# Optimization experiments

Hardware: AMD Instinct MI355X
Metric: run time of the kernel (lower is better)

Reference implementation:

```python
import jax, jax.numpy as jnp
import numpy as np
from jax import lax

# module hyperparams (from init_kwargs)
K = 7
STRIDE = 1
PAD = 3
DIL = 1


def setup_inputs() -> dict:
    key = jax.random.key(0)
    ks = jax.random.split(key, 5)
    B, Cin, Cout, L = 4, 256, 256, 8192
    x = jax.random.normal(ks[0], (B, Cin, L), jnp.float32)
    # main conv weight (Cout, Cin, K), kaiming-ish scale
    weight = jax.random.normal(ks[1], (Cout, Cin, K), jnp.float32) * (1.0 / np.sqrt(Cin * K))
    bias = jax.random.normal(ks[2], (Cout,), jnp.float32) * 0.01
    # offset conv: Conv1d(Cin -> K, kernel K); small values so sampling is perturbed but in-range
    offset_w = jax.random.normal(ks[3], (K, Cin, K), jnp.float32) * 0.01
    offset_b = jax.random.normal(ks[4], (K,), jnp.float32) * 0.01
    return {"x": x, "weight": weight, "bias": bias, "offset_w": offset_w, "offset_b": offset_b}


def reference(x, weight, bias, offset_w, offset_b):
    B, Cin, L = x.shape
    out_len = (L + 2 * PAD - DIL * (K - 1) - 1) // STRIDE + 1

    # offset conv: (B, Cin, L) -> (B, K, out_len)
    offsets = lax.conv_general_dilated(
        x, offset_w, window_strides=(STRIDE,), padding=[(PAD, PAD)],
        rhs_dilation=(DIL,), dimension_numbers=("NCH", "OIH", "NCH"))
    offsets = offsets + offset_b[None, :, None]
    offsets = jnp.transpose(offsets, (0, 2, 1))  # (B, out_len, K)

    # standard sampling locations (1, out_len, K), shifted by padding as in original
    p = jnp.arange(out_len, dtype=jnp.float32)[None, :, None] * STRIDE
    p_k = (jnp.arange(K, dtype=jnp.float32) - (K - 1) / 2.0) * DIL
    loc = p + p_k[None, None, :] + PAD + offsets  # (B, out_len, K)

    # linear interpolation (clamped endpoints, matching torch clamp order)
    x0 = jnp.floor(loc).astype(jnp.int32)
    x1 = x0 + 1
    x0c = jnp.clip(x0, 0, L - 1)
    x1c = jnp.clip(x1, 0, L - 1)
    wa = x1c.astype(jnp.float32) - loc  # weights use clamped indices, as original
    wb = loc - x0c.astype(jnp.float32)

    # gather: per batch, (Cin, L)[:, (out_len, K)] -> (Cin, out_len, K)
    gather = jax.vmap(lambda xb, ib: xb[:, ib])
    fa = gather(x, x0c)  # (B, Cin, out_len, K)
    fb = gather(x, x1c)
    interp = wa[:, None] * fa + wb[:, None] * fb  # (B, Cin, out_len, K)

    # einsum 'blki,oik->blo' with interp laid out as (B, i=Cin, l, k)
    out = jnp.einsum("bilk,oik->bol", interp, weight) + bias[None, :, None]
    return out
```

## Files before the change

kernel.cpp:

```cpp
#include <hip/hip_runtime.h>
#include <hip/hip_bf16.h>


#define B_    4
#define CIN   256
#define COUT  256
#define LEN   8192
#define KK    7
#define NTOT  (B_ * LEN)
#define QTOT  (CIN * KK)
#define LPITCH 232

typedef short s16x8 __attribute__((ext_vector_type(8)));
typedef int   s32x4 __attribute__((ext_vector_type(4)));
typedef float f32x4 __attribute__((ext_vector_type(4)));

static __device__ __forceinline__ unsigned f2bf(float f) {
  union { float f; unsigned u; } u; u.f = f;
  unsigned r = u.u + 0x7FFF + ((u.u >> 16) & 1);
  return r >> 16;
}

__global__ __launch_bounds__(256) void loc_partial(
    const float* __restrict__ X, const float* __restrict__ OW,
    float* __restrict__ Partial) {
  __shared__ float red[4][256][KK];

  const int t    = threadIdx.x;
  const int lane = t & 63;
  const int wu   = __builtin_amdgcn_readfirstlane(t >> 6);
  const int cg   = blockIdx.x >> 7;
  const int nb   = (blockIdx.x & 127) << 8;
  const int b    = nb >> 13;
  const int l0   = nb & (LEN - 1);

  float acc[KK][4];
#pragma unroll
  for (int k = 0; k < KK; ++k)
#pragma unroll
    for (int r = 0; r < 4; ++r) acc[k][r] = 0.0f;

#pragma unroll 2
  for (int ii = 0; ii < 16; ++ii) {
    const int i = cg * 64 + wu * 16 + ii;
    float owv[49];
#pragma unroll
    for (int k = 0; k < KK; ++k)
#pragma unroll
      for (int j = 0; j < KK; ++j)
        owv[k * 7 + j] = OW[(k * CIN + i) * KK + j];

    const float* xr = X + ((size_t)(b * CIN + i) << 13);
#pragma unroll
    for (int r = 0; r < 4; ++r) {
      const int lr = l0 + lane + 64 * r;
      float xv[KK];
#pragma unroll
      for (int j = 0; j < KK; ++j) {
        int pos = lr + j - 3;
        xv[j] = ((unsigned)pos < LEN) ? xr[pos] : 0.0f;
      }
#pragma unroll
      for (int k = 0; k < KK; ++k)
#pragma unroll
        for (int j = 0; j < KK; ++j)
          acc[k][r] += xv[j] * owv[k * 7 + j];
    }
  }

#pragma unroll
  for (int k = 0; k < KK; ++k)
#pragma unroll
    for (int r = 0; r < 4; ++r) red[wu][lane + 64 * r][k] = acc[k][r];
  __syncthreads();

#pragma unroll
  for (int k = 0; k < KK; ++k) {
    float s = red[0][t][k] + red[1][t][k] + red[2][t][k] + red[3][t][k];
    Partial[((size_t)(cg * 7 + k) << 15) + nb + t] = s;
  }
}

__global__ __launch_bounds__(256) void loc_reduce(
    const float* __restrict__ Partial, const float* __restrict__ OB,
    float* __restrict__ Loc) {
  int n = blockIdx.x * 256 + threadIdx.x;
  int l = n & (LEN - 1);
#pragma unroll
  for (int k = 0; k < KK; ++k) {
    float s = (float)(l + k) + OB[k];
#pragma unroll
    for (int cg = 0; cg < 4; ++cg)
      s += Partial[((size_t)(cg * 7 + k) << 15) + n];
    Loc[((size_t)k << 15) + n] = s;
  }
}

__global__ __launch_bounds__(256) void wt_build(
    const float* __restrict__ W, unsigned short* __restrict__ Wf) {
  __shared__ float Wl[16 * 32 * KK];
  const int t  = threadIdx.x;
  const int ot = blockIdx.x >> 3;
  const int c  = blockIdx.x & 7;

  for (int e = t; e < 16 * 32 * KK; e += 256) {
    int o = e / 224;
    int r = e - o * 224;
    Wl[e] = W[(size_t)(ot * 16 + o) * QTOT + c * 224 + r];
  }
  __syncthreads();

  const int lane = t & 63;
  const int sg   = t >> 6;
  const int ol   = lane & 15;
  const int ig   = lane >> 4;
  for (int s = sg; s < KK; s += 4) {
    s16x8 v;
#pragma unroll
    for (int j = 0; j < 8; ++j)
      v[j] = (short)f2bf(Wl[ol * 224 + (ig * 8 + j) * KK + s]);
    int f = (ot * 8 + c) * KK + s;
    *(s16x8*)(Wf + ((size_t)f << 9) + (lane << 3)) = v;
  }
}

__global__ __launch_bounds__(512, 4) void main_kernel(
    const float* __restrict__ X, const unsigned short* __restrict__ Wf,
    const float* __restrict__ Bias, const float* __restrict__ Loc,
    float* __restrict__ Out) {
  __shared__ unsigned short Il[2][64][LPITCH];

  const int t    = threadIdx.x;
  const int lane = t & 63;
  const int w    = t >> 6;
  const int n0   = blockIdx.x << 6;
  const int b    = n0 >> 13;
  const float* Xb = X + ((size_t)b << 21);

  const bool stager = (t < 448);
  const int nl = t & 63;
  const int kt = t >> 6;

  float c0 = 0.f, c1 = 0.f;
  const float* xp = Xb;
  if (stager) {
    float locv = Loc[((size_t)kt << 15) + n0 + nl];
    int x0  = (int)floorf(locv);
    int x0c = min(max(x0, 0), LEN - 1);
    int x1c = min(max(x0 + 1, 0), LEN - 1);
    float wa = (float)x1c - locv;
    float wb = locv - (float)x0c;
    bool hi = (x0 >= LEN - 1);
    bool lo = (x0 < 0);
    c0 = (hi ? 0.f : wa) + (lo ? wb : 0.f);
    c1 = (hi ? wa : 0.f) + (lo ? 0.f : wb);
    xp = Xb + min(max(x0, 0), LEN - 2);
  }

  f32x4 acc[2][4];
#pragma unroll
  for (int a = 0; a < 2; ++a)
#pragma unroll
    for (int cc = 0; cc < 4; ++cc) acc[a][cc] = (f32x4){0.f, 0.f, 0.f, 0.f};

  const int mrow = lane & 15;
  const int quad = lane >> 4;

  float f0[8], f1[8];

#define GATHER_Q(chunk, q)                                        \
  if (stager) {                                                   \
    _Pragma("unroll")                                             \
    for (int m = 0; m < 8; ++m) {                                 \
      const float* xr = xp + ((size_t)((chunk) * 32 + (q) * 8 + m) << 13); \
      f0[m] = xr[0];                                              \
      f1[m] = xr[1];                                              \
    }                                                             \
  }

#define CVT_Q(dst, q)                                             \
  if (stager) {                                                   \
    s32x4 vv;                                                     \
    _Pragma("unroll")                                             \
    for (int m = 0; m < 4; ++m) {                                 \
      float a = c0 * f0[2 * m]     + c1 * f1[2 * m];              \
      float d = c0 * f0[2 * m + 1] + c1 * f1[2 * m + 1];          \
      vv[m] = (int)(f2bf(a) | (f2bf(d) << 16));                   \
    }                                                             \
    *(s32x4*)((dst) + nl * LPITCH + kt * 32 + (q) * 8) = vv;      \
  }

#define AFL(ttv, sv)                                              \
  (*(const s16x8*)(Wf + ((size_t)(((w * 2 + (ttv)) * 8 + c) * KK + (sv)) << 9) + (lane << 3)))

#define MSTEP(sv, a0, a1) {                                                        \
    const s16x8 b0 = *(const s16x8*)(Icur + (mrow)      * LPITCH + (sv) * 32 + quad * 8); \
    const s16x8 b1 = *(const s16x8*)(Icur + (16 + mrow) * LPITCH + (sv) * 32 + quad * 8); \
    acc[0][0] = __builtin_amdgcn_mfma_f32_16x16x32_bf16(a0, b0, acc[0][0], 0, 0, 0); \
    acc[1][0] = __builtin_amdgcn_mfma_f32_16x16x32_bf16(a1, b0, acc[1][0], 0, 0, 0); \
    acc[0][1] = __builtin_amdgcn_mfma_f32_16x16x32_bf16(a0, b1, acc[0][1], 0, 0, 0); \
    acc[1][1] = __builtin_amdgcn_mfma_f32_16x16x32_bf16(a1, b1, acc[1][1], 0, 0, 0); \
    const s16x8 b2 = *(const s16x8*)(Icur + (32 + mrow) * LPITCH + (sv) * 32 + quad * 8); \
    const s16x8 b3 = *(const s16x8*)(Icur + (48 + mrow) * LPITCH + (sv) * 32 + quad * 8); \
    acc[0][2] = __builtin_amdgcn_mfma_f32_16x16x32_bf16(a0, b2, acc[0][2], 0, 0, 0); \
    acc[1][2] = __builtin_amdgcn_mfma_f32_16x16x32_bf16(a1, b2, acc[1][2], 0, 0, 0); \
    acc[0][3] = __builtin_amdgcn_mfma_f32_16x16x32_bf16(a0, b3, acc[0][3], 0, 0, 0); \
    acc[1][3] = __builtin_amdgcn_mfma_f32_16x16x32_bf16(a1, b3, acc[1][3], 0, 0, 0); \
  }

  {
    unsigned short* I0 = &Il[0][0][0];
    GATHER_Q(0, 0) CVT_Q(I0, 0)
    GATHER_Q(0, 1) CVT_Q(I0, 1)
    GATHER_Q(0, 2) CVT_Q(I0, 2)
    GATHER_Q(0, 3) CVT_Q(I0, 3)
  }
  __syncthreads();

  for (int c = 0; c < 8; ++c) {
    const int cur = c & 1;
    const unsigned short* Icur = &Il[cur][0][0];
    unsigned short*       Inxt = &Il[cur ^ 1][0][0];

    s16x8 afA[2][4];
#pragma unroll
    for (int tt = 0; tt < 2; ++tt)
#pragma unroll
      for (int s = 0; s < 4; ++s) afA[tt][s] = AFL(tt, s);
    __builtin_amdgcn_sched_barrier(0);

    if (c < 7) { GATHER_Q(c + 1, 0) }
    MSTEP(0, afA[0][0], afA[1][0])
    if (c < 7) { CVT_Q(Inxt, 0) GATHER_Q(c + 1, 1) }
    MSTEP(1, afA[0][1], afA[1][1])

    s16x8 afB[2][3];
#pragma unroll
    for (int tt = 0; tt < 2; ++tt)
#pragma unroll
      for (int s = 0; s < 3; ++s) afB[tt][s] = AFL(tt, 4 + s);
    __builtin_amdgcn_sched_barrier(0);

    if (c < 7) { CVT_Q(Inxt, 1) GATHER_Q(c + 1, 2) }
    MSTEP(2, afA[0][2], afA[1][2])
    if (c < 7) { CVT_Q(Inxt, 2) GATHER_Q(c + 1, 3) }
    MSTEP(3, afA[0][3], afA[1][3])
    if (c < 7) { CVT_Q(Inxt, 3) }
    MSTEP(4, afB[0][0], afB[1][0])
    MSTEP(5, afB[0][1], afB[1][1])
    MSTEP(6, afB[0][2], afB[1][2])
    if (c < 7) __syncthreads();
  }
#undef GATHER_Q
#undef CVT_Q
#undef AFL
#undef MSTEP

  const int lbase = (n0 & (LEN - 1)) + mrow;
#pragma unroll
  for (int tt = 0; tt < 2; ++tt) {
    const int obase = (w * 2 + tt) * 16 + quad * 4;
#pragma unroll
    for (int r = 0; r < 4; ++r) {
      const int o = obase + r;
      const float bv = Bias[o];
      float* orow = Out + (((size_t)(b * COUT + o)) << 13) + lbase;
#pragma unroll
      for (int nt = 0; nt < 4; ++nt)
        orow[nt * 16] = acc[tt][nt][r] + bv;
    }
  }
}

extern "C" void kernel_launch(void* const* d_in, const int* in_sizes, int n_in,
                              void* d_out, int out_size, void* d_ws, size_t ws_size,
                              hipStream_t stream) {
  const float* X    = (const float*)d_in[0];
  const float* W    = (const float*)d_in[1];
  const float* Bias = (const float*)d_in[2];
  const float* OW   = (const float*)d_in[3];
  const float* OB   = (const float*)d_in[4];
  float* Out = (float*)d_out;

  float* Loc = (float*)d_ws;
  unsigned short* Wf = (unsigned short*)(Loc + (size_t)NTOT * KK);
  float* Partial = (float*)(Wf + (size_t)COUT * QTOT);

  loc_partial<<<4 * 128, 256, 0, stream>>>(X, OW, Partial);
  loc_reduce<<<NTOT / 256, 256, 0, stream>>>(Partial, OB, Loc);
  wt_build<<<128, 256, 0, stream>>>(W, Wf);
  main_kernel<<<NTOT / 64, 512, 0, stream>>>(X, Wf, Bias, Loc, Out);
}
```

Before: 168.8 us.

## Double-buffer gather registers, halve loc_partial tile, use packed bf16 convert

The main kernel's gather staging now uses two register sets, so the next quarter's global loads are issued a full MFMA step before the previous quarter is converted and stored to LDS. This hides gather latency better at the cost of more VGPRs. loc_partial now processes 128 positions per block with twice as many blocks, which raises parallelism for the offset conv but reuses each weight load over fewer positions. The manual bf16 rounding is replaced with the packed float2-to-bfloat162 intrinsic.

```diff
diff --git a/kernel.cpp b/kernel.cpp
--- a/kernel.cpp
+++ b/kernel.cpp
@@ -1,5 +1,6 @@
 #include <hip/hip_runtime.h>
 #include <hip/hip_bf16.h>
+#include <string.h>
 
 
 #define B_    4
@@ -21,24 +22,31 @@
   return r >> 16;
 }
 
+static __device__ __forceinline__ int pack_bf16(float a, float d) {
+  __hip_bfloat162 h = __float22bfloat162_rn(make_float2(a, d));
+  int r;
+  __builtin_memcpy(&r, &h, 4);
+  return r;
+}
+
 __global__ __launch_bounds__(256) void loc_partial(
     const float* __restrict__ X, const float* __restrict__ OW,
     float* __restrict__ Partial) {
-  __shared__ float red[4][256][KK];
+  __shared__ float red[4][128][KK];
 
   const int t    = threadIdx.x;
   const int lane = t & 63;
   const int wu   = __builtin_amdgcn_readfirstlane(t >> 6);
-  const int cg   = blockIdx.x >> 7;
-  const int nb   = (blockIdx.x & 127) << 8;
+  const int cg   = blockIdx.x >> 8;
+  const int nb   = (blockIdx.x & 255) << 7;
   const int b    = nb >> 13;
   const int l0   = nb & (LEN - 1);
 
-  float acc[KK][4];
+  float acc[KK][2];
 #pragma unroll
   for (int k = 0; k < KK; ++k)
 #pragma unroll
-    for (int r = 0; r < 4; ++r) acc[k][r] = 0.0f;
+    for (int r = 0; r < 2; ++r) acc[k][r] = 0.0f;
 
 #pragma unroll 2
   for (int ii = 0; ii < 16; ++ii) {
@@ -52,7 +60,7 @@
 
     const float* xr = X + ((size_t)(b * CIN + i) << 13);
 #pragma unroll
-    for (int r = 0; r < 4; ++r) {
+    for (int r = 0; r < 2; ++r) {
       const int lr = l0 + lane + 64 * r;
       float xv[KK];
 #pragma unroll
@@ -71,13 +79,15 @@
 #pragma unroll
   for (int k = 0; k < KK; ++k)
 #pragma unroll
-    for (int r = 0; r < 4; ++r) red[wu][lane + 64 * r][k] = acc[k][r];
+    for (int r = 0; r < 2; ++r) red[wu][lane + 64 * r][k] = acc[k][r];
   __syncthreads();
 
-#pragma unroll
-  for (int k = 0; k < KK; ++k) {
-    float s = red[0][t][k] + red[1][t][k] + red[2][t][k] + red[3][t][k];
-    Partial[((size_t)(cg * 7 + k) << 15) + nb + t] = s;
+  if (t < 128) {
+#pragma unroll
+    for (int k = 0; k < KK; ++k) {
+      float s = red[0][t][k] + red[1][t][k] + red[2][t][k] + red[3][t][k];
+      Partial[((size_t)(cg * 7 + k) << 15) + nb + t] = s;
+    }
   }
 }
 
@@ -166,26 +176,26 @@
   const int mrow = lane & 15;
   const int quad = lane >> 4;
 
-  float f0[8], f1[8];
-
-#define GATHER_Q(chunk, q)                                        \
+  float f0[2][8], f1[2][8];
+
+#define GATHER_Q(chunk, q, rs)                                    \
   if (stager) {                                                   \
     _Pragma("unroll")                                             \
     for (int m = 0; m < 8; ++m) {                                 \
       const float* xr = xp + ((size_t)((chunk) * 32 + (q) * 8 + m) << 13); \
-      f0[m] = xr[0];                                              \
-      f1[m] = xr[1];                                              \
+      f0[rs][m] = xr[0];                                          \
+      f1[rs][m] = xr[1];                                          \
     }                                                             \
   }
 
-#define CVT_Q(dst, q)                                             \
+#define CVT_Q(dst, q, rs)                                         \
   if (stager) {                                                   \
     s32x4 vv;                                                     \
     _Pragma("unroll")                                             \
     for (int m = 0; m < 4; ++m) {                                 \
-      float a = c0 * f0[2 * m]     + c1 * f1[2 * m];              \
-      float d = c0 * f0[2 * m + 1] + c1 * f1[2 * m + 1];          \
-      vv[m] = (int)(f2bf(a) | (f2bf(d) << 16));                   \
+      float a = c0 * f0[rs][2 * m]     + c1 * f1[rs][2 * m];      \
+      float d = c0 * f0[rs][2 * m + 1] + c1 * f1[rs][2 * m + 1];  \
+      vv[m] = pack_bf16(a, d);                                    \
     }                                                             \
     *(s32x4*)((dst) + nl * LPITCH + kt * 32 + (q) * 8) = vv;      \
   }
@@ -210,10 +220,10 @@
 
   {
     unsigned short* I0 = &Il[0][0][0];
-    GATHER_Q(0, 0) CVT_Q(I0, 0)
-    GATHER_Q(0, 1) CVT_Q(I0, 1)
-    GATHER_Q(0, 2) CVT_Q(I0, 2)
-    GATHER_Q(0, 3) CVT_Q(I0, 3)
+    GATHER_Q(0, 0, 0) CVT_Q(I0, 0, 0)
+    GATHER_Q(0, 1, 0) CVT_Q(I0, 1, 0)
+    GATHER_Q(0, 2, 0) CVT_Q(I0, 2, 0)
+    GATHER_Q(0, 3, 0) CVT_Q(I0, 3, 0)
   }
   __syncthreads();
 
@@ -229,10 +239,11 @@
       for (int s = 0; s < 4; ++s) afA[tt][s] = AFL(tt, s);
     __builtin_amdgcn_sched_barrier(0);
 
-    if (c < 7) { GATHER_Q(c + 1, 0) }
+    if (c < 7) { GATHER_Q(c + 1, 0, 0) }
     MSTEP(0, afA[0][0], afA[1][0])
-    if (c < 7) { CVT_Q(Inxt, 0) GATHER_Q(c + 1, 1) }
+    if (c < 7) { GATHER_Q(c + 1, 1, 1) }
     MSTEP(1, afA[0][1], afA[1][1])
+    if (c < 7) { CVT_Q(Inxt, 0, 0) }
 
     s16x8 afB[2][3];
 #pragma unroll
@@ -241,15 +252,19 @@
       for (int s = 0; s < 3; ++s) afB[tt][s] = AFL(tt, 4 + s);
     __builtin_amdgcn_sched_barrier(0);
 
-    if (c < 7) { CVT_Q(Inxt, 1) GATHER_Q(c + 1, 2) }
     MSTEP(2, afA[0][2], afA[1][2])
-    if (c < 7) { CVT_Q(Inxt, 2) GATHER_Q(c + 1, 3) }
+    if (c < 7) { GATHER_Q(c + 1, 2, 0) }
     MSTEP(3, afA[0][3], afA[1][3])
-    if (c < 7) { CVT_Q(Inxt, 3) }
+    if (c < 7) { CVT_Q(Inxt, 1, 1) }
     MSTEP(4, afB[0][0], afB[1][0])
+    if (c < 7) { GATHER_Q(c + 1, 3, 1) }
     MSTEP(5, afB[0][1], afB[1][1])
+    if (c < 7) { CVT_Q(Inxt, 2, 0) }
     MSTEP(6, afB[0][2], afB[1][2])
-    if (c < 7) __syncthreads();
+    if (c < 7) {
+      CVT_Q(Inxt, 3, 1)
+      __syncthreads();
+    }
   }
 #undef GATHER_Q
 #undef CVT_Q
@@ -286,7 +301,7 @@
   unsigned short* Wf = (unsigned short*)(Loc + (size_t)NTOT * KK);
   float* Partial = (float*)(Wf + (size_t)COUT * QTOT);
 
-  loc_partial<<<4 * 128, 256, 0, stream>>>(X, OW, Partial);
+  loc_partial<<<4 * 256, 256, 0, stream>>>(X, OW, Partial);
   loc_reduce<<<NTOT / 256, 256, 0, stream>>>(Partial, OB, Loc);
   wt_build<<<128, 256, 0, stream>>>(W, Wf);
   main_kernel<<<NTOT / 64, 512, 0, stream>>>(X, Wf, Bias, Loc, Out);
```

New measurement: 188.4 us. 1.12x slower.
